# Performance work log

Measured on AMD Instinct MI355X. Metric: run time of the kernel, lower is better.

The kernel has to match this reference:

```python
import jax, jax.numpy as jnp
import numpy as np

B, L, H, HKV, D, HID, FFN = 32, 4096, 32, 2, 128, 4096, 13696
ROT = 64  # rotary_dim = kv_channels // 2 (GLM style)
EPS = 1e-5


def setup_inputs() -> dict:
    key = jax.random.key(0)
    ks = jax.random.split(key, 9)
    s = 0.02
    return {
        "hidden_states": jax.random.normal(ks[0], (B, HID), jnp.float32),
        "context_lens": jax.random.randint(ks[1], (B,), 1, L - 1, dtype=jnp.int32),
        "key_cache": jax.random.normal(ks[2], (B, L, HKV, D), jnp.float32),
        "value_cache": jax.random.normal(ks[3], (B, L, HKV, D), jnp.float32),
        "w_ln1": jnp.ones((HID,), jnp.float32),
        "w_ln2": jnp.ones((HID,), jnp.float32),
        "w_qkv": jax.random.normal(ks[4], (HID, H * D + 2 * HKV * D), jnp.float32) * s,
        "b_qkv": jax.random.normal(ks[5], (H * D + 2 * HKV * D,), jnp.float32) * s,
        "w_dense": jax.random.normal(ks[6], (H * D, HID), jnp.float32) * s,
        "w_h4h": jax.random.normal(ks[7], (HID, 2 * FFN), jnp.float32) * s,
        "w_4hh": jax.random.normal(ks[8], (FFN, HID), jnp.float32) * s,
    }


def rmsnorm(x, w):
    v = jnp.mean(x.astype(jnp.float32) ** 2, axis=-1, keepdims=True)
    return (w * (x * jax.lax.rsqrt(v + EPS))).astype(x.dtype)


def apply_rope(x, pos):
    # x: [B, heads, D]; GPT-J interleaved rotary on first ROT dims (glm=True)
    half = ROT // 2
    inv = 1.0 / (10000.0 ** (jnp.arange(half, dtype=jnp.float32) / half))
    f = pos.astype(jnp.float32)[:, None] * inv[None, :]          # [B, half]
    cos, sin = jnp.cos(f)[:, None, :], jnp.sin(f)[:, None, :]    # [B,1,half]
    xr, xp = x[..., :ROT], x[..., ROT:]
    x1, x2 = xr[..., 0::2], xr[..., 1::2]
    rot = jnp.stack([x1 * cos - x2 * sin, x2 * cos + x1 * sin], axis=-1).reshape(xr.shape)
    return jnp.concatenate([rot, xp], axis=-1)


def reference(hidden_states, context_lens, key_cache, value_cache,
              w_ln1, w_ln2, w_qkv, b_qkv, w_dense, w_h4h, w_4hh):
    # input RMSNorm
    ln1 = rmsnorm(hidden_states, w_ln1)
    # fused QKV projection (add_qkv_bias=True)
    qkv = ln1 @ w_qkv + b_qkv
    q, k, v = jnp.split(qkv, [H * D, H * D + HKV * D], axis=-1)
    q = apply_rope(q.reshape(B, H, D), context_lens)
    k = apply_rope(k.reshape(B, HKV, D), context_lens)
    v = v.reshape(B, HKV, D)
    # write new K/V into the paged cache at this token's slot
    kc = key_cache.at[jnp.arange(B), context_lens].set(k)
    vc = value_cache.at[jnp.arange(B), context_lens].set(v)
    # GQA attention: 32 q heads grouped over 2 kv heads
    qg = q.reshape(B, HKV, H // HKV, D)
    scores = jnp.einsum('bghd,blgd->bghl', qg, kc) * (D ** -0.5)
    mask = jnp.arange(L)[None, :] <= context_lens[:, None]       # [B, L]
    scores = jnp.where(mask[:, None, None, :], scores, -jnp.inf)
    p = jax.nn.softmax(scores, axis=-1)
    ctx = jnp.einsum('bghl,blgd->bghd', p, vc).reshape(B, H * D)
    attn_out = ctx @ w_dense                                     # add_bias_linear=False
    x = hidden_states + attn_out                                  # residual pre-LN
    ln2 = rmsnorm(x, w_ln2)
    g, u = jnp.split(ln2 @ w_h4h, 2, axis=-1)
    out = (jax.nn.silu(g) * u) @ w_4hh + x
    return out
```

## Files before the change

### kernel.cpp

```cpp
#include <hip/hip_runtime.h>
#include <hip/hip_bf16.h>

#define B_    32
#define L_    4096
#define H_    32
#define HKV_  2
#define GQ_   16
#define D_    128
#define HID_  4096
#define FFN_  13696
#define NQKV_ 4608
#define ROT_  64
#define EPS_  1e-5f

#define WAVE_POS_ 128
#define NSPLIT_   32

#define KS_QKV_  16
#define KS_DEN_  24
#define KS_H4H_  3
#define KS_4HH_  24

typedef __attribute__((ext_vector_type(8))) __bf16 bf16x8;
typedef __attribute__((ext_vector_type(4))) float  f32x4;

__device__ __forceinline__ void gl_lds16(const float* g, float* l) {
    __builtin_amdgcn_global_load_lds((const __attribute__((address_space(1))) void*)g,
                                     (__attribute__((address_space(3))) void*)l, 16, 0, 0);
}

__global__ __launch_bounds__(1024) void rmsnorm1_k(const float* __restrict__ x,
                                                   const float* __restrict__ w,
                                                   __bf16* __restrict__ out)
{
    int b = blockIdx.x;
    const float* row = x + (size_t)b * HID_;
    float vals[4];
    float ss = 0.f;
#pragma unroll
    for (int i = 0; i < 4; ++i) {
        vals[i] = row[threadIdx.x + i * 1024];
        ss += vals[i] * vals[i];
    }
#pragma unroll
    for (int m = 1; m < 64; m <<= 1) ss += __shfl_xor(ss, m);
    __shared__ float wred[16];
    if ((threadIdx.x & 63) == 0) wred[threadIdx.x >> 6] = ss;
    __syncthreads();
    ss = 0.f;
#pragma unroll
    for (int wv = 0; wv < 16; ++wv) ss += wred[wv];
    float rs = rsqrtf(ss / HID_ + EPS_);
#pragma unroll
    for (int i = 0; i < 4; ++i) {
        int idx = threadIdx.x + i * 1024;
        out[(size_t)b * HID_ + idx] = (__bf16)(w[idx] * vals[i] * rs);
    }
}

template<int K, int N, int KSPLIT>
__global__ __launch_bounds__(256) void gemm16(const __bf16* __restrict__ A,
                                              const float* __restrict__ W,
                                              float* __restrict__ Cp)
{
    static_assert(K % 32 == 0, "K");
    constexpr int ksteps = K / 32;
    const int lane = threadIdx.x & 63;
    const int wid  = threadIdx.x >> 6;
    const int n0   = blockIdx.x * 128;
    const int cw   = wid * 32;
    const int r    = lane & 15;
    const int g4   = lane >> 4;
    const int s0   = (ksteps * (int)blockIdx.y) / KSPLIT;
    const int s1   = (ksteps * (int)(blockIdx.y + 1)) / KSPLIT;

    __shared__ float tiles[3][32][128];

    const int rhalf = lane >> 5;
    const int mslot = lane & 31;
    auto stage = [&](int s, float* dst) {
        if (s >= s1) return;
#pragma unroll
        for (int it = 0; it < 4; ++it) {
            int row  = wid * 8 + it * 2 + rhalf;
            int gcol = ((((mslot >> 1) ^ (row >> 3)) << 3) | ((mslot & 1) << 2));
            const float* src = W + (size_t)(s * 32 + row) * N + n0 + gcol;
            gl_lds16(src, dst + (size_t)(wid * 8 + it * 2) * 128);
        }
    };

    f32x4 acc00 = {0.f,0.f,0.f,0.f}, acc01 = acc00, acc10 = acc00, acc11 = acc00;
    const __bf16* a0p = A + (size_t)r * K;
    const __bf16* a1p = A + (size_t)(r + 16) * K;

    stage(s0,     &tiles[0][0][0]);
    stage(s0 + 1, &tiles[1][0][0]);

    const int c0 = cw + r, c1 = cw + r + 16;
    const int i0 = (((c0 >> 3) ^ g4) << 3) | (c0 & 7);
    const int i1 = (((c1 >> 3) ^ g4) << 3) | (c1 & 7);

    int bufc = 0;
    for (int s = s0; s < s1; ++s) {
        if (s + 1 < s1) asm volatile("s_waitcnt vmcnt(4)" ::: "memory");
        else            asm volatile("s_waitcnt vmcnt(0)" ::: "memory");
        __builtin_amdgcn_s_barrier();
        __builtin_amdgcn_sched_barrier(0);
        int bs = bufc + 2; if (bs >= 3) bs -= 3;
        stage(s + 2, &tiles[bs][0][0]);

        bf16x8 av0 = *(const bf16x8*)(a0p + s * 32 + g4 * 8);
        bf16x8 av1 = *(const bf16x8*)(a1p + s * 32 + g4 * 8);
        const float (*tile)[128] = tiles[bufc];
        bf16x8 b0f, b1f;
#pragma unroll
        for (int j = 0; j < 8; ++j) {
            b0f[j] = (__bf16)tile[g4 * 8 + j][i0];
            b1f[j] = (__bf16)tile[g4 * 8 + j][i1];
        }
        acc00 = __builtin_amdgcn_mfma_f32_16x16x32_bf16(av0, b0f, acc00, 0, 0, 0);
        acc10 = __builtin_amdgcn_mfma_f32_16x16x32_bf16(av1, b0f, acc10, 0, 0, 0);
        acc01 = __builtin_amdgcn_mfma_f32_16x16x32_bf16(av0, b1f, acc01, 0, 0, 0);
        acc11 = __builtin_amdgcn_mfma_f32_16x16x32_bf16(av1, b1f, acc11, 0, 0, 0);
        bufc = (bufc + 1 < 3) ? bufc + 1 : 0;
    }

    float* cp = Cp + ((size_t)blockIdx.y * 32) * N + n0 + cw;
#pragma unroll
    for (int i = 0; i < 4; ++i) {
        cp[(size_t)(g4 * 4 + i) * N + r]           = acc00[i];
        cp[(size_t)(g4 * 4 + i) * N + r + 16]      = acc01[i];
        cp[(size_t)(16 + g4 * 4 + i) * N + r]      = acc10[i];
        cp[(size_t)(16 + g4 * 4 + i) * N + r + 16] = acc11[i];
    }
}

__global__ __launch_bounds__(1024) void qkv_epi_k(const float* __restrict__ part,
                                                  const float* __restrict__ bias,
                                                  const int* __restrict__ ctxl,
                                                  __bf16* __restrict__ qbf,
                                                  float* __restrict__ knew,
                                                  float* __restrict__ vnew)
{
    __shared__ float rowv[1152];
    __shared__ float cs[32], sn[32];
    int b = blockIdx.x, base = blockIdx.y * 1152;
    int pos = ctxl[b];
    if (threadIdx.x < 32) {
        int t = threadIdx.x;
        float inv = powf(10000.f, -(float)t * (1.0f / 32.0f));
        float f = (float)pos * inv;
        float sv, cv; sincosf(f, &sv, &cv);
        cs[t] = cv; sn[t] = sv;
    }
    for (int i0 = threadIdx.x; i0 < 1152; i0 += 1024) {
        int i = base + i0;
        float v = bias[i];
#pragma unroll
        for (int p = 0; p < KS_QKV_; ++p) v += part[((size_t)p * B_ + b) * NQKV_ + i];
        rowv[i0] = v;
    }
    __syncthreads();
    const float qscale = 0.08838834764831845f;
    for (int i0 = threadIdx.x; i0 < 1152; i0 += 1024) {
        int i = base + i0;
        int d = i & 127;
        if (i < HID_) {
            float o;
            if (d < ROT_) {
                int t = d >> 1;
                float cv = cs[t], sv = sn[t];
                float x1 = rowv[(i & ~1) - base], x2 = rowv[(i | 1) - base];
                o = (d & 1) ? (x2 * cv + x1 * sv) : (x1 * cv - x2 * sv);
            } else o = rowv[i0];
            qbf[(size_t)b * HID_ + i] = (__bf16)(o * qscale);
        } else {
            int j = i - HID_;
            if (j < HKV_ * D_) {
                float o;
                if (d < ROT_) {
                    int t = d >> 1;
                    float cv = cs[t], sv = sn[t];
                    float x1 = rowv[(i & ~1) - base], x2 = rowv[(i | 1) - base];
                    o = (d & 1) ? (x2 * cv + x1 * sv) : (x1 * cv - x2 * sv);
                } else o = rowv[i0];
                knew[(size_t)b * HKV_ * D_ + j] = o;
            } else {
                vnew[(size_t)b * HKV_ * D_ + (j - HKV_ * D_)] = rowv[i0];
            }
        }
    }
}

__global__ __launch_bounds__(256) void attn_k(const float* __restrict__ kc,
                                              const float* __restrict__ vc,
                                              const float* __restrict__ knew,
                                              const float* __restrict__ vnew,
                                              const __bf16* __restrict__ qbf,
                                              const int* __restrict__ ctxl,
                                              float* __restrict__ part)
{
    const int bg  = blockIdx.x;
    const int b   = bg >> 1, g = bg & 1;
    const int wid = threadIdx.x >> 6;
    const int split = blockIdx.y * 4 + wid;
    const int ctx = ctxl[b];
    const int p0  = split * WAVE_POS_;
    __shared__ __bf16 plds_all[4][16][40];
    if (p0 > ctx) return;
    const int pend = min(p0 + WAVE_POS_ - 1, ctx);
    const int lane = threadIdx.x & 63;
    const int r = lane & 15, g4 = lane >> 4;

    bf16x8 qf[4];
    {
        const __bf16* qp = qbf + (size_t)b * HID_ + (g * GQ_ + r) * D_ + g4 * 8;
#pragma unroll
        for (int kk = 0; kk < 4; ++kk) qf[kk] = *(const bf16x8*)(qp + kk * 32);
    }
    f32x4 acc[8];
#pragma unroll
    for (int dt = 0; dt < 8; ++dt) acc[dt] = (f32x4){0.f,0.f,0.f,0.f};
    float m_run[4], l_run[4];
#pragma unroll
    for (int i = 0; i < 4; ++i) { m_run[i] = -1e30f; l_run[i] = 0.f; }

    auto plds = plds_all[wid];
    const float* kbase = kc + ((size_t)b * L_ * HKV_ + g) * D_;
    const float* vbase = vc + ((size_t)b * L_ * HKV_ + g) * D_;
    const float* knp = knew + (size_t)(b * HKV_ + g) * D_;
    const float* vnp = vnew + (size_t)(b * HKV_ + g) * D_;

    for (int pc = p0; pc <= pend; pc += 32) {
        f32x4 sf[2];
#pragma unroll
        for (int pt = 0; pt < 2; ++pt) {
            int pos = pc + pt * 16 + r;
            const float* krow = (pos == ctx) ? knp : kbase + (size_t)pos * (HKV_ * D_);
            f32x4 s = {0.f,0.f,0.f,0.f};
#pragma unroll
            for (int kk = 0; kk < 4; ++kk) {
                const float4* kp = (const float4*)(krow + kk * 32 + g4 * 8);
                float4 fa = kp[0], fb = kp[1];
                bf16x8 kf = { (__bf16)fa.x, (__bf16)fa.y, (__bf16)fa.z, (__bf16)fa.w,
                              (__bf16)fb.x, (__bf16)fb.y, (__bf16)fb.z, (__bf16)fb.w };
                s = __builtin_amdgcn_mfma_f32_16x16x32_bf16(qf[kk], kf, s, 0, 0, 0);
            }
            sf[pt] = s;
        }
#pragma unroll
        for (int pt = 0; pt < 2; ++pt) {
            int pos = pc + pt * 16 + r;
            if (pos > ctx) {
#pragma unroll
                for (int i = 0; i < 4; ++i) sf[pt][i] = -1e30f;
            }
        }
#pragma unroll
        for (int i = 0; i < 4; ++i) {
            float mv = fmaxf(sf[0][i], sf[1][i]);
            mv = fmaxf(mv, __shfl_xor(mv, 1));
            mv = fmaxf(mv, __shfl_xor(mv, 2));
            mv = fmaxf(mv, __shfl_xor(mv, 4));
            mv = fmaxf(mv, __shfl_xor(mv, 8));
            float mnew = fmaxf(m_run[i], mv);
            float sc = __expf(m_run[i] - mnew);
            l_run[i] *= sc;
            m_run[i] = mnew;
#pragma unroll
            for (int dt = 0; dt < 8; ++dt) acc[dt][i] *= sc;
        }
#pragma unroll
        for (int pt = 0; pt < 2; ++pt) {
#pragma unroll
            for (int i = 0; i < 4; ++i) {
                float e = __expf(sf[pt][i] - m_run[i]);
                l_run[i] += e;
                plds[g4 * 4 + i][pt * 16 + r] = (__bf16)e;
            }
        }
        asm volatile("s_waitcnt lgkmcnt(0)" ::: "memory");
        __builtin_amdgcn_sched_barrier(0);
        bf16x8 pa = *(const bf16x8*)&plds[r][g4 * 8];
        const float* vrows[8];
#pragma unroll
        for (int j = 0; j < 8; ++j) {
            int pos = pc + g4 * 8 + j;
            vrows[j] = (pos == ctx) ? vnp : vbase + (size_t)pos * (HKV_ * D_);
        }
#pragma unroll
        for (int dt = 0; dt < 8; ++dt) {
            bf16x8 vf;
#pragma unroll
            for (int j = 0; j < 8; ++j) vf[j] = (__bf16)vrows[j][dt * 16 + r];
            acc[dt] = __builtin_amdgcn_mfma_f32_16x16x32_bf16(pa, vf, acc[dt], 0, 0, 0);
        }
        asm volatile("s_waitcnt lgkmcnt(0)" ::: "memory");
        __builtin_amdgcn_sched_barrier(0);
    }
#pragma unroll
    for (int i = 0; i < 4; ++i) {
        float lv = l_run[i];
        lv += __shfl_xor(lv, 1);
        lv += __shfl_xor(lv, 2);
        lv += __shfl_xor(lv, 4);
        lv += __shfl_xor(lv, 8);
        l_run[i] = lv;
    }
    float* pb = part + ((size_t)bg * NSPLIT_ + split) * 16 * 130;
#pragma unroll
    for (int dt = 0; dt < 8; ++dt)
#pragma unroll
        for (int i = 0; i < 4; ++i)
            pb[(g4 * 4 + i) * 130 + dt * 16 + r] = acc[dt][i];
    if (r == 0) {
#pragma unroll
        for (int i = 0; i < 4; ++i) {
            pb[(g4 * 4 + i) * 130 + 128] = m_run[i];
            pb[(g4 * 4 + i) * 130 + 129] = l_run[i];
        }
    }
}

__global__ __launch_bounds__(1024) void attn_comb_k(const float* __restrict__ part,
                                                    const int* __restrict__ ctxl,
                                                    __bf16* __restrict__ ctxb)
{
    int bg = blockIdx.x;
    int c  = blockIdx.y;
    int b = bg >> 1, g = bg & 1;
    int ctx = ctxl[b];
    int ns = ctx / WAVE_POS_ + 1;
    const float* pb = part + (size_t)bg * NSPLIT_ * 16 * 130;
    __shared__ float mlm[NSPLIT_][16], wgt[NSPLIT_][16];
    __shared__ float Mh[16], Ih[16];
    int t = threadIdx.x;
    if (t < NSPLIT_ * 16) {
        int s = t >> 4, h = t & 15;
        mlm[s][h] = pb[(s * 16 + h) * 130 + 128];
        wgt[s][h] = pb[(s * 16 + h) * 130 + 129];
    }
    __syncthreads();
    if (t < 16) {
        int h = t;
        float M = -1e30f;
        for (int s = 0; s < ns; ++s) M = fmaxf(M, mlm[s][h]);
        float den = 0.f;
        for (int s = 0; s < ns; ++s) den += __expf(mlm[s][h] - M) * wgt[s][h];
        Mh[h] = M; Ih[h] = 1.f / den;
    }
    __syncthreads();
    if (t < NSPLIT_ * 16) {
        int s = t >> 4, h = t & 15;
        wgt[s][h] = __expf(mlm[s][h] - Mh[h]) * Ih[h];
    }
    __syncthreads();
    int h = t >> 6, dd = (t & 63) + c * 64;
    float o = 0.f;
    for (int s = 0; s < ns; ++s)
        o += wgt[s][h] * pb[(s * 16 + h) * 130 + dd];
    ctxb[(size_t)b * HID_ + (g * GQ_ + h) * D_ + dd] = (__bf16)o;
}

__global__ __launch_bounds__(1024) void dense_red_k(const float* __restrict__ hidden,
                                                    const float* __restrict__ partd,
                                                    float* __restrict__ xout,
                                                    float* __restrict__ ssq)
{
    int b = blockIdx.x;
    int i = blockIdx.y * 1024 + threadIdx.x;
    float v = hidden[(size_t)b * HID_ + i];
#pragma unroll
    for (int p = 0; p < KS_DEN_; ++p) v += partd[((size_t)p * B_ + b) * HID_ + i];
    xout[(size_t)b * HID_ + i] = v;
    float ss = v * v;
#pragma unroll
    for (int m = 1; m < 64; m <<= 1) ss += __shfl_xor(ss, m);
    __shared__ float wred[16];
    if ((threadIdx.x & 63) == 0) wred[threadIdx.x >> 6] = ss;
    __syncthreads();
    if (threadIdx.x == 0) {
        float s = 0.f;
#pragma unroll
        for (int wv = 0; wv < 16; ++wv) s += wred[wv];
        ssq[b * 4 + blockIdx.y] = s;
    }
}

__global__ __launch_bounds__(1024) void rms2_k(const float* __restrict__ xbuf,
                                               const float* __restrict__ ssq,
                                               const float* __restrict__ wln2,
                                               __bf16* __restrict__ a2)
{
    int b = blockIdx.x;
    float ss = ssq[b * 4] + ssq[b * 4 + 1] + ssq[b * 4 + 2] + ssq[b * 4 + 3];
    float rs = rsqrtf(ss / HID_ + EPS_);
#pragma unroll
    for (int it = 0; it < 4; ++it) {
        int i = threadIdx.x + it * 1024;
        a2[(size_t)b * HID_ + i] = (__bf16)(wln2[i] * xbuf[(size_t)b * HID_ + i] * rs);
    }
}

__global__ __launch_bounds__(256) void act_k(const float* __restrict__ gu,
                                             __bf16* __restrict__ act)
{
    int i = blockIdx.x * 256 + threadIdx.x;
    int b = blockIdx.y;
    if (i < FFN_) {
        float gv = 0.f, uv = 0.f;
#pragma unroll
        for (int p = 0; p < KS_H4H_; ++p) {
            const float* gp = gu + ((size_t)p * B_ + b) * 2 * FFN_;
            gv += gp[i];
            uv += gp[FFN_ + i];
        }
        float s = gv / (1.f + __expf(-gv));
        act[(size_t)b * FFN_ + i] = (__bf16)(s * uv);
    }
}

__global__ __launch_bounds__(256) void out_epi_k(const float* __restrict__ x,
                                                 const float* __restrict__ part4,
                                                 float* __restrict__ out)
{
    int i = blockIdx.x * 256 + threadIdx.x;
    float v = x[i];
#pragma unroll
    for (int p = 0; p < KS_4HH_; ++p) v += part4[(size_t)p * (B_ * HID_) + i];
    out[i] = v;
}

extern "C" void kernel_launch(void* const* d_in, const int* in_sizes, int n_in,
                              void* d_out, int out_size, void* d_ws, size_t ws_size,
                              hipStream_t stream)
{
    const float* hidden  = (const float*)d_in[0];
    const int*   ctxl    = (const int*)d_in[1];
    const float* kcache  = (const float*)d_in[2];
    const float* vcache  = (const float*)d_in[3];
    const float* w_ln1   = (const float*)d_in[4];
    const float* w_ln2   = (const float*)d_in[5];
    const float* w_qkv   = (const float*)d_in[6];
    const float* b_qkv   = (const float*)d_in[7];
    const float* w_dense = (const float*)d_in[8];
    const float* w_h4h   = (const float*)d_in[9];
    const float* w_4hh   = (const float*)d_in[10];
    float* out = (float*)d_out;

    char* ws = (char*)d_ws;
    size_t off = 0;
    auto alloc = [&](size_t bytes) -> void* {
        void* p = ws + off;
        off += (bytes + 255) & ~(size_t)255;
        return p;
    };
    __bf16* a0    = (__bf16*)alloc((size_t)B_ * HID_ * 2);
    float*  partq = (float*) alloc((size_t)KS_QKV_ * B_ * NQKV_ * 4);
    __bf16* qbf   = (__bf16*)alloc((size_t)B_ * HID_ * 2);
    float*  knew  = (float*) alloc((size_t)B_ * HKV_ * D_ * 4);
    float*  vnew  = (float*) alloc((size_t)B_ * HKV_ * D_ * 4);
    float*  apart = (float*) alloc((size_t)B_ * HKV_ * NSPLIT_ * 16 * 130 * 4);
    __bf16* ctxb  = (__bf16*)alloc((size_t)B_ * HID_ * 2);
    float*  partd = (float*) alloc((size_t)KS_DEN_ * B_ * HID_ * 4);
    float*  xbuf  = (float*) alloc((size_t)B_ * HID_ * 4);
    float*  ssq   = (float*) alloc((size_t)B_ * 4 * 4);
    __bf16* a2    = (__bf16*)alloc((size_t)B_ * HID_ * 2);
    float*  gu    = (float*) alloc((size_t)KS_H4H_ * B_ * 2 * FFN_ * 4);
    __bf16* actb  = (__bf16*)alloc((size_t)B_ * FFN_ * 2);
    float*  part4 = (float*) alloc((size_t)KS_4HH_ * B_ * HID_ * 4);
    (void)ws_size; (void)in_sizes; (void)n_in; (void)out_size;

    hipLaunchKernelGGL(rmsnorm1_k, dim3(B_), dim3(1024), 0, stream, hidden, w_ln1, a0);
    hipLaunchKernelGGL((gemm16<HID_, NQKV_, KS_QKV_>), dim3(NQKV_ / 128, KS_QKV_), dim3(256), 0, stream, a0, w_qkv, partq);
    hipLaunchKernelGGL(qkv_epi_k, dim3(B_, 4), dim3(1024), 0, stream, partq, b_qkv, ctxl, qbf, knew, vnew);
    hipLaunchKernelGGL(attn_k, dim3(B_ * HKV_, NSPLIT_ / 4), dim3(256), 0, stream,
                       kcache, vcache, knew, vnew, qbf, ctxl, apart);
    hipLaunchKernelGGL(attn_comb_k, dim3(B_ * HKV_, 2), dim3(1024), 0, stream, apart, ctxl, ctxb);
    hipLaunchKernelGGL((gemm16<HID_, HID_, KS_DEN_>), dim3(HID_ / 128, KS_DEN_), dim3(256), 0, stream, ctxb, w_dense, partd);
    hipLaunchKernelGGL(dense_red_k, dim3(B_, 4), dim3(1024), 0, stream, hidden, partd, xbuf, ssq);
    hipLaunchKernelGGL(rms2_k, dim3(B_), dim3(1024), 0, stream, xbuf, ssq, w_ln2, a2);
    hipLaunchKernelGGL((gemm16<HID_, 2 * FFN_, KS_H4H_>), dim3(2 * FFN_ / 128, KS_H4H_), dim3(256), 0, stream, a2, w_h4h, gu);
    hipLaunchKernelGGL(act_k, dim3((FFN_ + 255) / 256, B_), dim3(256), 0, stream, gu, actb);
    hipLaunchKernelGGL((gemm16<FFN_, HID_, KS_4HH_>), dim3(HID_ / 128, KS_4HH_), dim3(256), 0, stream, actb, w_4hh, part4);
    hipLaunchKernelGGL(out_epi_k, dim3(B_ * HID_ / 256), dim3(256), 0, stream, xbuf, part4, out);
}
```

Before: 261.9 us.

## Stage V tiles through swizzled LDS with coalesced loads issued before QK

The attention kernel now loads each 32-row V tile with coalesced float4 global loads at the top of the loop iteration, before the QK MFMAs, and writes it to a per-wave swizzled LDS buffer. The transposed scalar gather for the PV MFMA then reads from LDS instead of making strided global loads. K fragments are also converted to bf16 ahead of the QK MFMAs so more loads are in flight at once. The cost is about 67KB of extra LDS per block and higher register pressure from the 16 float4 V registers, both of which can lower occupancy.

```diff
diff --git a/kernel.cpp b/kernel.cpp
--- a/kernel.cpp
+++ b/kernel.cpp
@@ -207,10 +207,13 @@
     const int ctx = ctxl[b];
     const int p0  = split * WAVE_POS_;
     __shared__ __bf16 plds_all[4][16][40];
+    __shared__ __align__(16) float vlds_all[4][32][132];
     if (p0 > ctx) return;
     const int pend = min(p0 + WAVE_POS_ - 1, ctx);
     const int lane = threadIdx.x & 63;
     const int r = lane & 15, g4 = lane >> 4;
+    const int vrow2 = lane >> 5;
+    const int vcol  = (lane & 31) * 4;
 
     bf16x8 qf[4];
     {
@@ -226,26 +229,41 @@
     for (int i = 0; i < 4; ++i) { m_run[i] = -1e30f; l_run[i] = 0.f; }
 
     auto plds = plds_all[wid];
+    float (*vlds)[132] = vlds_all[wid];
     const float* kbase = kc + ((size_t)b * L_ * HKV_ + g) * D_;
     const float* vbase = vc + ((size_t)b * L_ * HKV_ + g) * D_;
     const float* knp = knew + (size_t)(b * HKV_ + g) * D_;
     const float* vnp = vnew + (size_t)(b * HKV_ + g) * D_;
 
     for (int pc = p0; pc <= pend; pc += 32) {
-        f32x4 sf[2];
+        float4 vreg[16];
+#pragma unroll
+        for (int t = 0; t < 16; ++t) {
+            int row = t * 2 + vrow2;
+            int pos = pc + row;
+            const float* vr = (pos == ctx) ? vnp : vbase + (size_t)pos * (HKV_ * D_);
+            vreg[t] = *(const float4*)(vr + vcol);
+        }
+        bf16x8 kfr[2][4];
 #pragma unroll
         for (int pt = 0; pt < 2; ++pt) {
             int pos = pc + pt * 16 + r;
             const float* krow = (pos == ctx) ? knp : kbase + (size_t)pos * (HKV_ * D_);
-            f32x4 s = {0.f,0.f,0.f,0.f};
 #pragma unroll
             for (int kk = 0; kk < 4; ++kk) {
                 const float4* kp = (const float4*)(krow + kk * 32 + g4 * 8);
                 float4 fa = kp[0], fb = kp[1];
-                bf16x8 kf = { (__bf16)fa.x, (__bf16)fa.y, (__bf16)fa.z, (__bf16)fa.w,
-                              (__bf16)fb.x, (__bf16)fb.y, (__bf16)fb.z, (__bf16)fb.w };
-                s = __builtin_amdgcn_mfma_f32_16x16x32_bf16(qf[kk], kf, s, 0, 0, 0);
+                kfr[pt][kk] = (bf16x8){ (__bf16)fa.x, (__bf16)fa.y, (__bf16)fa.z, (__bf16)fa.w,
+                                        (__bf16)fb.x, (__bf16)fb.y, (__bf16)fb.z, (__bf16)fb.w };
             }
+        }
+        f32x4 sf[2];
+#pragma unroll
+        for (int pt = 0; pt < 2; ++pt) {
+            f32x4 s = {0.f,0.f,0.f,0.f};
+#pragma unroll
+            for (int kk = 0; kk < 4; ++kk)
+                s = __builtin_amdgcn_mfma_f32_16x16x32_bf16(qf[kk], kfr[pt][kk], s, 0, 0, 0);
             sf[pt] = s;
         }
 #pragma unroll
@@ -279,20 +297,21 @@
                 plds[g4 * 4 + i][pt * 16 + r] = (__bf16)e;
             }
         }
+#pragma unroll
+        for (int t = 0; t < 16; ++t) {
+            int row = t * 2 + vrow2;
+            int c2  = vcol ^ (((row >> 3) & 1) << 4);
+            *(float4*)&vlds[row][c2] = vreg[t];
+        }
         asm volatile("s_waitcnt lgkmcnt(0)" ::: "memory");
         __builtin_amdgcn_sched_barrier(0);
         bf16x8 pa = *(const bf16x8*)&plds[r][g4 * 8];
-        const float* vrows[8];
-#pragma unroll
-        for (int j = 0; j < 8; ++j) {
-            int pos = pc + g4 * 8 + j;
-            vrows[j] = (pos == ctx) ? vnp : vbase + (size_t)pos * (HKV_ * D_);
-        }
 #pragma unroll
         for (int dt = 0; dt < 8; ++dt) {
             bf16x8 vf;
-#pragma unroll
-            for (int j = 0; j < 8; ++j) vf[j] = (__bf16)vrows[j][dt * 16 + r];
+            int cread = (dt * 16 + r) ^ ((g4 & 1) << 4);
+#pragma unroll
+            for (int j = 0; j < 8; ++j) vf[j] = (__bf16)vlds[g4 * 8 + j][cread];
             acc[dt] = __builtin_amdgcn_mfma_f32_16x16x32_bf16(pa, vf, acc[dt], 0, 0, 0);
         }
         asm volatile("s_waitcnt lgkmcnt(0)" ::: "memory");
```

Result: slower. 274.1 us (+4.6%).

## Replace split-K partial buffers with atomic accumulation into pre-initialized outputs

Applied to the files above, without the earlier changes.

Each split-K GEMM now atomically adds its tile into a single destination buffer instead of writing per-split partial slabs. The destinations are pre-seeded by earlier kernels: bias for QKV, the residual for dense, zero for gate/up, and x into the final output. This removes the separate reduction reads and the final out_epi kernel. The cost is float atomic traffic, with up to 24-way contention per element, and summation order that is no longer deterministic.

```diff
diff --git a/kernel.cpp b/kernel.cpp
--- a/kernel.cpp
+++ b/kernel.cpp
@@ -31,9 +31,13 @@
 
 __global__ __launch_bounds__(1024) void rmsnorm1_k(const float* __restrict__ x,
                                                    const float* __restrict__ w,
-                                                   __bf16* __restrict__ out)
+                                                   const float* __restrict__ bias,
+                                                   __bf16* __restrict__ out,
+                                                   float* __restrict__ qacc)
 {
     int b = blockIdx.x;
+    for (int i = threadIdx.x; i < NQKV_; i += 1024)
+        qacc[(size_t)b * NQKV_ + i] = bias[i];
     const float* row = x + (size_t)b * HID_;
     float vals[4];
     float ss = 0.f;
@@ -61,7 +65,7 @@
 template<int K, int N, int KSPLIT>
 __global__ __launch_bounds__(256) void gemm16(const __bf16* __restrict__ A,
                                               const float* __restrict__ W,
-                                              float* __restrict__ Cp)
+                                              float* __restrict__ C)
 {
     static_assert(K % 32 == 0, "K");
     constexpr int ksteps = K / 32;
@@ -125,18 +129,17 @@
         bufc = (bufc + 1 < 3) ? bufc + 1 : 0;
     }
 
-    float* cp = Cp + ((size_t)blockIdx.y * 32) * N + n0 + cw;
+    float* cp = C + n0 + cw;
 #pragma unroll
     for (int i = 0; i < 4; ++i) {
-        cp[(size_t)(g4 * 4 + i) * N + r]           = acc00[i];
-        cp[(size_t)(g4 * 4 + i) * N + r + 16]      = acc01[i];
-        cp[(size_t)(16 + g4 * 4 + i) * N + r]      = acc10[i];
-        cp[(size_t)(16 + g4 * 4 + i) * N + r + 16] = acc11[i];
-    }
-}
-
-__global__ __launch_bounds__(1024) void qkv_epi_k(const float* __restrict__ part,
-                                                  const float* __restrict__ bias,
+        unsafeAtomicAdd(&cp[(size_t)(g4 * 4 + i) * N + r],           acc00[i]);
+        unsafeAtomicAdd(&cp[(size_t)(g4 * 4 + i) * N + r + 16],      acc01[i]);
+        unsafeAtomicAdd(&cp[(size_t)(16 + g4 * 4 + i) * N + r],      acc10[i]);
+        unsafeAtomicAdd(&cp[(size_t)(16 + g4 * 4 + i) * N + r + 16], acc11[i]);
+    }
+}
+
+__global__ __launch_bounds__(1024) void qkv_epi_k(const float* __restrict__ qacc,
                                                   const int* __restrict__ ctxl,
                                                   __bf16* __restrict__ qbf,
                                                   float* __restrict__ knew,
@@ -153,13 +156,8 @@
         float sv, cv; sincosf(f, &sv, &cv);
         cs[t] = cv; sn[t] = sv;
     }
-    for (int i0 = threadIdx.x; i0 < 1152; i0 += 1024) {
-        int i = base + i0;
-        float v = bias[i];
-#pragma unroll
-        for (int p = 0; p < KS_QKV_; ++p) v += part[((size_t)p * B_ + b) * NQKV_ + i];
-        rowv[i0] = v;
-    }
+    for (int i0 = threadIdx.x; i0 < 1152; i0 += 1024)
+        rowv[i0] = qacc[(size_t)b * NQKV_ + base + i0];
     __syncthreads();
     const float qscale = 0.08838834764831845f;
     for (int i0 = threadIdx.x; i0 < 1152; i0 += 1024) {
@@ -324,11 +322,17 @@
 
 __global__ __launch_bounds__(1024) void attn_comb_k(const float* __restrict__ part,
                                                     const int* __restrict__ ctxl,
-                                                    __bf16* __restrict__ ctxb)
+                                                    const float* __restrict__ hidden,
+                                                    __bf16* __restrict__ ctxb,
+                                                    float* __restrict__ dacc)
 {
     int bg = blockIdx.x;
     int c  = blockIdx.y;
     int b = bg >> 1, g = bg & 1;
+    {
+        int seg = (g * 2 + c) * 1024 + threadIdx.x;
+        dacc[(size_t)b * HID_ + seg] = hidden[(size_t)b * HID_ + seg];
+    }
     int ctx = ctxl[b];
     int ns = ctx / WAVE_POS_ + 1;
     const float* pb = part + (size_t)bg * NSPLIT_ * 16 * 130;
@@ -362,17 +366,16 @@
     ctxb[(size_t)b * HID_ + (g * GQ_ + h) * D_ + dd] = (__bf16)o;
 }
 
-__global__ __launch_bounds__(1024) void dense_red_k(const float* __restrict__ hidden,
-                                                    const float* __restrict__ partd,
+__global__ __launch_bounds__(1024) void dense_red_k(const float* __restrict__ dacc,
                                                     float* __restrict__ xout,
+                                                    float* __restrict__ outbuf,
                                                     float* __restrict__ ssq)
 {
     int b = blockIdx.x;
     int i = blockIdx.y * 1024 + threadIdx.x;
-    float v = hidden[(size_t)b * HID_ + i];
-#pragma unroll
-    for (int p = 0; p < KS_DEN_; ++p) v += partd[((size_t)p * B_ + b) * HID_ + i];
+    float v = dacc[(size_t)b * HID_ + i];
     xout[(size_t)b * HID_ + i] = v;
+    outbuf[(size_t)b * HID_ + i] = v;
     float ss = v * v;
 #pragma unroll
     for (int m = 1; m < 64; m <<= 1) ss += __shfl_xor(ss, m);
@@ -390,9 +393,12 @@
 __global__ __launch_bounds__(1024) void rms2_k(const float* __restrict__ xbuf,
                                                const float* __restrict__ ssq,
                                                const float* __restrict__ wln2,
-                                               __bf16* __restrict__ a2)
+                                               __bf16* __restrict__ a2,
+                                               float* __restrict__ guacc)
 {
     int b = blockIdx.x;
+    for (int i = threadIdx.x; i < 2 * FFN_; i += 1024)
+        guacc[(size_t)b * 2 * FFN_ + i] = 0.f;
     float ss = ssq[b * 4] + ssq[b * 4 + 1] + ssq[b * 4 + 2] + ssq[b * 4 + 3];
     float rs = rsqrtf(ss / HID_ + EPS_);
 #pragma unroll
@@ -402,33 +408,18 @@
     }
 }
 
-__global__ __launch_bounds__(256) void act_k(const float* __restrict__ gu,
+__global__ __launch_bounds__(256) void act_k(const float* __restrict__ guacc,
                                              __bf16* __restrict__ act)
 {
     int i = blockIdx.x * 256 + threadIdx.x;
     int b = blockIdx.y;
     if (i < FFN_) {
-        float gv = 0.f, uv = 0.f;
-#pragma unroll
-        for (int p = 0; p < KS_H4H_; ++p) {
-            const float* gp = gu + ((size_t)p * B_ + b) * 2 * FFN_;
-            gv += gp[i];
-            uv += gp[FFN_ + i];
-        }
+        const float* gp = guacc + (size_t)b * 2 * FFN_;
+        float gv = gp[i];
+        float uv = gp[FFN_ + i];
         float s = gv / (1.f + __expf(-gv));
         act[(size_t)b * FFN_ + i] = (__bf16)(s * uv);
     }
-}
-
-__global__ __launch_bounds__(256) void out_epi_k(const float* __restrict__ x,
-                                                 const float* __restrict__ part4,
-                                                 float* __restrict__ out)
-{
-    int i = blockIdx.x * 256 + threadIdx.x;
-    float v = x[i];
-#pragma unroll
-    for (int p = 0; p < KS_4HH_; ++p) v += part4[(size_t)p * (B_ * HID_) + i];
-    out[i] = v;
 }
 
 extern "C" void kernel_launch(void* const* d_in, const int* in_sizes, int n_in,
@@ -456,32 +447,30 @@
         return p;
     };
     __bf16* a0    = (__bf16*)alloc((size_t)B_ * HID_ * 2);
-    float*  partq = (float*) alloc((size_t)KS_QKV_ * B_ * NQKV_ * 4);
+    float*  qacc  = (float*) alloc((size_t)B_ * NQKV_ * 4);
     __bf16* qbf   = (__bf16*)alloc((size_t)B_ * HID_ * 2);
     float*  knew  = (float*) alloc((size_t)B_ * HKV_ * D_ * 4);
     float*  vnew  = (float*) alloc((size_t)B_ * HKV_ * D_ * 4);
     float*  apart = (float*) alloc((size_t)B_ * HKV_ * NSPLIT_ * 16 * 130 * 4);
     __bf16* ctxb  = (__bf16*)alloc((size_t)B_ * HID_ * 2);
-    float*  partd = (float*) alloc((size_t)KS_DEN_ * B_ * HID_ * 4);
+    float*  dacc  = (float*) alloc((size_t)B_ * HID_ * 4);
     float*  xbuf  = (float*) alloc((size_t)B_ * HID_ * 4);
     float*  ssq   = (float*) alloc((size_t)B_ * 4 * 4);
     __bf16* a2    = (__bf16*)alloc((size_t)B_ * HID_ * 2);
-    float*  gu    = (float*) alloc((size_t)KS_H4H_ * B_ * 2 * FFN_ * 4);
+    float*  guacc = (float*) alloc((size_t)B_ * 2 * FFN_ * 4);
     __bf16* actb  = (__bf16*)alloc((size_t)B_ * FFN_ * 2);
-    float*  part4 = (float*) alloc((size_t)KS_4HH_ * B_ * HID_ * 4);
     (void)ws_size; (void)in_sizes; (void)n_in; (void)out_size;
 
-    hipLaunchKernelGGL(rmsnorm1_k, dim3(B_), dim3(1024), 0, stream, hidden, w_ln1, a0);
-    hipLaunchKernelGGL((gemm16<HID_, NQKV_, KS_QKV_>), dim3(NQKV_ / 128, KS_QKV_), dim3(256), 0, stream, a0, w_qkv, partq);
-    hipLaunchKernelGGL(qkv_epi_k, dim3(B_, 4), dim3(1024), 0, stream, partq, b_qkv, ctxl, qbf, knew, vnew);
+    hipLaunchKernelGGL(rmsnorm1_k, dim3(B_), dim3(1024), 0, stream, hidden, w_ln1, b_qkv, a0, qacc);
+    hipLaunchKernelGGL((gemm16<HID_, NQKV_, KS_QKV_>), dim3(NQKV_ / 128, KS_QKV_), dim3(256), 0, stream, a0, w_qkv, qacc);
+    hipLaunchKernelGGL(qkv_epi_k, dim3(B_, 4), dim3(1024), 0, stream, qacc, ctxl, qbf, knew, vnew);
     hipLaunchKernelGGL(attn_k, dim3(B_ * HKV_, NSPLIT_ / 4), dim3(256), 0, stream,
                        kcache, vcache, knew, vnew, qbf, ctxl, apart);
-    hipLaunchKernelGGL(attn_comb_k, dim3(B_ * HKV_, 2), dim3(1024), 0, stream, apart, ctxl, ctxb);
-    hipLaunchKernelGGL((gemm16<HID_, HID_, KS_DEN_>), dim3(HID_ / 128, KS_DEN_), dim3(256), 0, stream, ctxb, w_dense, partd);
-    hipLaunchKernelGGL(dense_red_k, dim3(B_, 4), dim3(1024), 0, stream, hidden, partd, xbuf, ssq);
-    hipLaunchKernelGGL(rms2_k, dim3(B_), dim3(1024), 0, stream, xbuf, ssq, w_ln2, a2);
-    hipLaunchKernelGGL((gemm16<HID_, 2 * FFN_, KS_H4H_>), dim3(2 * FFN_ / 128, KS_H4H_), dim3(256), 0, stream, a2, w_h4h, gu);
-    hipLaunchKernelGGL(act_k, dim3((FFN_ + 255) / 256, B_), dim3(256), 0, stream, gu, actb);
-    hipLaunchKernelGGL((gemm16<FFN_, HID_, KS_4HH_>), dim3(HID_ / 128, KS_4HH_), dim3(256), 0, stream, actb, w_4hh, part4);
-    hipLaunchKernelGGL(out_epi_k, dim3(B_ * HID_ / 256), dim3(256), 0, stream, xbuf, part4, out);
-}
+    hipLaunchKernelGGL(attn_comb_k, dim3(B_ * HKV_, 2), dim3(1024), 0, stream, apart, ctxl, hidden, ctxb, dacc);
+    hipLaunchKernelGGL((gemm16<HID_, HID_, KS_DEN_>), dim3(HID_ / 128, KS_DEN_), dim3(256), 0, stream, ctxb, w_dense, dacc);
+    hipLaunchKernelGGL(dense_red_k, dim3(B_, 4), dim3(1024), 0, stream, dacc, xbuf, out, ssq);
+    hipLaunchKernelGGL(rms2_k, dim3(B_), dim3(1024), 0, stream, xbuf, ssq, w_ln2, a2, guacc);
+    hipLaunchKernelGGL((gemm16<HID_, 2 * FFN_, KS_H4H_>), dim3(2 * FFN_ / 128, KS_H4H_), dim3(256), 0, stream, a2, w_h4h, guacc);
+    hipLaunchKernelGGL(act_k, dim3((FFN_ + 255) / 256, B_), dim3(256), 0, stream, guacc, actb);
+    hipLaunchKernelGGL((gemm16<FFN_, HID_, KS_4HH_>), dim3(HID_ / 128, KS_4HH_), dim3(256), 0, stream, actb, w_4hh, out);
+}
```

New measurement: 261.9 us (median of 2 runs). Within noise of the previous version (+0.0%).
